# Kernel optimization log

Hardware: AMD Instinct MI355X
Metric: run time of the kernel (lower is better)

The kernel has to match this reference:

```python
import jax, jax.numpy as jnp
import numpy as np

B, T, S, H, E, V, NUM_OOV = 32, 32, 100, 512, 300, 45000, 10
INF = 1e12


def setup_inputs() -> dict:
    key = jax.random.key(0)
    ks = jax.random.split(key, 24)
    def n(k, shape, s=0.02):
        return jax.random.normal(k, shape, jnp.float32) * s
    return dict(
        trg_seq=jax.random.randint(ks[0], (B, T), 0, V),
        ext_src_seq=jax.random.randint(ks[1], (B, S), 0, V + NUM_OOV),
        h0=n(ks[2], (1, B, H), 0.1),
        c0=n(ks[3], (1, B, H), 0.1),
        tree_output=n(ks[4], (B, S, H), 1.0),
        tree_enc_states=n(ks[5], (1, B, H), 0.1),
        encoder_outputs=n(ks[6], (B, S, H), 1.0),
        encoder_mask=jnp.zeros((B, S), bool),
        embedding=n(ks[7], (V, E)),
        W_enc=n(ks[8], (2 * H, H)), b_enc=jnp.zeros((H,), jnp.float32),
        W_red=n(ks[9], (E + H, E)), b_red=jnp.zeros((E,), jnp.float32),
        W_ih=n(ks[10], (E, 4 * H)), W_hh=n(ks[11], (H, 4 * H)),
        b_ih=jnp.zeros((4 * H,), jnp.float32), b_hh=jnp.zeros((4 * H,), jnp.float32),
        W_cat=n(ks[12], (2 * H, H)), b_cat=jnp.zeros((H,), jnp.float32),
        W_out=n(ks[13], (H, V)), b_out=jnp.zeros((V,), jnp.float32),
    )


def reference(trg_seq, ext_src_seq, h0, c0, tree_output, tree_enc_states,
              encoder_outputs, encoder_mask, embedding, W_enc, b_enc,
              W_red, b_red, W_ih, W_hh, b_ih, b_hh, W_cat, b_cat, W_out, b_out):
    # encoder features: [B,S,2H] -> [B,S,H]
    memories = jnp.concatenate([tree_output, encoder_outputs], axis=-1) @ W_enc + b_enc
    rows = jnp.arange(B)[:, None]  # for per-row scatter-max
    Vext = V + NUM_OOV

    def step(carry, y):
        h, c, ctx = carry  # h,c: [B,H], ctx: [B,H]
        emb = embedding[y]                                   # [B,E]
        x = jnp.concatenate([emb, ctx], axis=-1) @ W_red + b_red  # [B,E]
        gates = x @ W_ih + h @ W_hh + (b_ih + b_hh)          # [B,4H]
        i, f, g, o = jnp.split(gates, 4, axis=-1)            # torch gate order i,f,g,o
        c_new = jax.nn.sigmoid(f) * c + jax.nn.sigmoid(i) * jnp.tanh(g)
        h_new = jax.nn.sigmoid(o) * jnp.tanh(c_new)
        energy = jnp.einsum('bh,bsh->bs', h_new, memories)   # [B,S]
        energy = jnp.where(encoder_mask, -INF, energy)
        attn = jax.nn.softmax(energy, axis=-1)
        ctx_new = jnp.einsum('bs,bsh->bh', attn, memories)   # [B,H]
        z = jnp.tanh(jnp.concatenate([h_new, ctx_new], axis=-1) @ W_cat + b_cat)
        logit = z @ W_out + b_out                            # [B,V]
        # pointer copy mechanism: scatter-max of energies into extended vocab
        ext = jnp.concatenate([logit, jnp.zeros((B, NUM_OOV), logit.dtype)], axis=-1)
        scat = jnp.full((B, Vext), -INF, logit.dtype).at[rows, ext_src_seq].max(energy)
        scat = jnp.where(scat == -INF, 0.0, scat)
        out = ext + scat
        out = jnp.where(out == 0.0, -INF, out)
        return (h_new, c_new, ctx_new), out

    init = (h0[0], c0[0], jnp.zeros((B, H), memories.dtype))
    _, logits = jax.lax.scan(step, init, trg_seq.T)  # [T,B,Vext]
    return jnp.transpose(logits, (1, 0, 2))          # [B,T,Vext]
```

## Files before the change

kernel.cpp:

```cpp
#include <hip/hip_runtime.h>
#include <hip/hip_bf16.h>
#include <stdint.h>

typedef __hip_bfloat16 bf16;
typedef __attribute__((ext_vector_type(8))) short short8;
typedef __attribute__((ext_vector_type(4))) float f32x4;

#define INFV 1e12f

constexpr int Vv = 45000;
constexpr int VE = 45010;

static __device__ __forceinline__ float bf2f(unsigned short u){
  union{ unsigned int i; float f; } w; w.i = ((unsigned int)u) << 16; return w.f;
}
static __device__ __forceinline__ unsigned short f2bf(float x){
  union { __hip_bfloat16 h; unsigned short u; } w; w.h = __float2bfloat16(x); return w.u;
}

template<bool ABF16, bool TANHOUT>
__launch_bounds__(256)
__global__ void k_gemm(const void* __restrict__ Ap, const void* __restrict__ Ap2, int Ksplit,
                       const float* __restrict__ Bp, const float* __restrict__ bias,
                       void* __restrict__ Cp, int M, int N, int K)
{
  __shared__ float As[16][68];
  __shared__ float Bs[16][68];
  int tid = threadIdx.x;
  int tx = tid & 15, ty = tid >> 4;
  int m0 = blockIdx.y * 64, n0 = blockIdx.x * 64;
  float acc[4][4] = {};
  for (int kc = 0; kc < K; kc += 16){
    for (int idx = tid; idx < 64*16; idx += 256){
      int r = idx >> 4, c = idx & 15;
      int gr = m0 + r, gk = kc + c;
      float v = 0.f;
      if (gr < M && gk < K){
        if (ABF16)            v = bf2f(((const unsigned short*)Ap)[(size_t)gr*K + gk]);
        else if (gk < Ksplit) v = ((const float*)Ap )[(size_t)gr*Ksplit + gk];
        else                  v = ((const float*)Ap2)[(size_t)gr*(K - Ksplit) + (gk - Ksplit)];
      }
      As[c][r] = v;
    }
    for (int idx = tid; idx < 16*64; idx += 256){
      int r = idx >> 6, c = idx & 63;
      int gk = kc + r, gn = n0 + c;
      Bs[r][c] = (gk < K && gn < N) ? Bp[(size_t)gk*N + gn] : 0.f;
    }
    __syncthreads();
    #pragma unroll
    for (int kk = 0; kk < 16; ++kk){
      float a[4], b[4];
      #pragma unroll
      for (int i = 0; i < 4; ++i) a[i] = As[kk][ty*4 + i];
      #pragma unroll
      for (int j = 0; j < 4; ++j) b[j] = Bs[kk][tx*4 + j];
      #pragma unroll
      for (int i = 0; i < 4; ++i)
        #pragma unroll
        for (int j = 0; j < 4; ++j) acc[i][j] = fmaf(a[i], b[j], acc[i][j]);
    }
    __syncthreads();
  }
  for (int i = 0; i < 4; ++i){
    int gr = m0 + ty*4 + i; if (gr >= M) continue;
    for (int j = 0; j < 4; ++j){
      int gn = n0 + tx*4 + j; if (gn >= N) continue;
      float v = acc[i][j] + (bias ? bias[gn] : 0.f);
      if (TANHOUT) ((unsigned short*)Cp)[(size_t)gr*N + gn] = f2bf(tanhf(v));
      else         ((float*)Cp)[(size_t)gr*N + gn] = v;
    }
  }
}

__global__ void k_cvt(const float* __restrict__ src, unsigned short* __restrict__ dst, int n){
  int i = blockIdx.x*256 + threadIdx.x;
  if (i < n) dst[i] = f2bf(src[i]);
}

__global__ void k_gather(const int* __restrict__ trg, const float* __restrict__ emb,
                         float* __restrict__ EmbA){
  int i = blockIdx.x*256 + threadIdx.x;
  if (i >= 1024*300) return;
  int r = i / 300, e = i - r*300;
  EmbA[i] = emb[(size_t)trg[r]*300 + e];
}

__global__ void k_bsum(const float* __restrict__ a, const float* __restrict__ b,
                       float* __restrict__ o){
  int i = blockIdx.x*256 + threadIdx.x;
  if (i < 2048) o[i] = a[i] + b[i];
}

__global__ void k_wgt(const float* __restrict__ Wf, const float* __restrict__ W_hh,
                      unsigned short* __restrict__ WgT){
  int idx = blockIdx.x*256 + threadIdx.x;
  if (idx >= 2048*1024) return;
  int cp = idx >> 10, k = idx & 1023;
  int c = (cp & 3)*512 + (cp >> 2);
  float v = (k < 512) ? Wf[(size_t)k*2048 + c] : W_hh[(size_t)(k-512)*2048 + c];
  WgT[idx] = f2bf(v);
}

__launch_bounds__(256)
__global__ void k_wot(const float* __restrict__ W_out, unsigned short* __restrict__ WoT){
  __shared__ float tl[64][65];
  int n0 = blockIdx.x * 64;
  int k0 = blockIdx.y * 64;
  int tid = threadIdx.x;
  for (int idx = tid; idx < 64*64; idx += 256){
    int r = idx >> 6, c = idx & 63;
    int gn = n0 + c;
    tl[r][c] = (gn < Vv) ? W_out[(size_t)(k0 + r)*Vv + gn] : 0.f;
  }
  __syncthreads();
  for (int idx = tid; idx < 64*64; idx += 256){
    int r = idx >> 6, c = idx & 63;
    WoT[(size_t)(n0 + r)*512 + k0 + c] = f2bf(tl[c][r]);
  }
}

__global__ void k_init(const float* __restrict__ h0, const float* __restrict__ c0,
                       unsigned short* __restrict__ HCa, float* __restrict__ Cst){
  int i = blockIdx.x*256 + threadIdx.x;
  if (i < 32*1024){
    int b = i >> 10, k = i & 1023;
    HCa[i] = (k < 512) ? f2bf(0.f) : f2bf(h0[b*512 + (k - 512)]);
  }
  if (i < 32*512) Cst[i] = c0[i];
}

__launch_bounds__(256, 1)
__global__ void k_gates(const unsigned short* __restrict__ WgT,
                        const unsigned short* __restrict__ HCprev,
                        unsigned short* __restrict__ HCnext,
                        float* __restrict__ C_state,
                        const float* __restrict__ G1,
                        unsigned short* __restrict__ HCz,
                        int t)
{
  __shared__ char Bsm[64*272];
  int tid = threadIdx.x;
  int lane = tid & 63, w2 = tid >> 6;
  int blk = blockIdx.x;
  int l15 = lane & 15, lh = lane >> 4;
  f32x4 zero = {0.f,0.f,0.f,0.f};
  f32x4 acc0 = zero, acc1 = zero;
  const char* Ab = (const char*)HCprev;

  for (int kc = 0; kc < 1024; kc += 128){
    #pragma unroll
    for (int call = 0; call < 4; ++call){
      int o = call*4096 + tid*16;
      int r = o >> 8, cb = o & 255;
      short8 v = *(const short8*)((const char*)WgT + (size_t)(blk*64 + r)*2048 + kc*2 + cb);
      *(short8*)(Bsm + r*272 + cb) = v;
    }
    __syncthreads();
    #pragma unroll
    for (int ks = 0; ks < 4; ++ks){
      short8 a0 = *(const short8*)(Ab + (size_t)l15*2048      + (kc + ks*32)*2 + lh*16);
      short8 a1 = *(const short8*)(Ab + (size_t)(l15+16)*2048 + (kc + ks*32)*2 + lh*16);
      int br = w2*16 + l15;
      short8 bfr = *(const short8*)(Bsm + br*272 + ks*64 + lh*16);
      acc0 = __builtin_amdgcn_mfma_f32_16x16x32_bf16(a0, bfr, acc0, 0, 0, 0);
      acc1 = __builtin_amdgcn_mfma_f32_16x16x32_bf16(a1, bfr, acc1, 0, 0, 0);
    }
    __syncthreads();
  }

  int cg = blk*64 + w2*16 + l15;
  int hfull = cg >> 2, q = cg & 3;
  #pragma unroll
  for (int f = 0; f < 2; ++f){
    #pragma unroll
    for (int j = 0; j < 4; ++j){
      int b = f*16 + 4*lh + j;
      float g = (f ? acc1[j] : acc0[j]) + G1[((size_t)b*32 + t)*2048 + q*512 + hfull];
      float x1 = (q == 2) ? tanhf(g) : 1.f/(1.f + expf(-g));
      float xg = __shfl_xor(x1, 2);
      float xf = __shfl_xor(x1, 1);
      float xo = __shfl_xor(x1, 3);
      if (q == 0){
        float co = C_state[b*512 + hfull];
        float cn = xf*co + x1*xg;
        float hn = xo * tanhf(cn);
        C_state[b*512 + hfull] = cn;
        unsigned short hb = f2bf(hn);
        HCnext[b*1024 + 512 + hfull] = hb;
        HCz[((size_t)b*32 + t)*1024 + hfull] = hb;
      }
    }
  }
}

__launch_bounds__(256, 1)
__global__ void k_attn(const unsigned short* __restrict__ memB,
                       const unsigned char* __restrict__ emask,
                       unsigned short* __restrict__ HCnext,
                       unsigned short* __restrict__ HCz,
                       float* __restrict__ Esave,
                       int t)
{
  int b = blockIdx.x;
  int tid = threadIdx.x, lane = tid & 63, w = tid >> 6;
  __shared__ float E_s[100];
  __shared__ float attn_s[100];
  float hreg[8];
  {
    short8 hv = *(const short8*)(HCnext + b*1024 + 512 + lane*8);
    #pragma unroll
    for (int i = 0; i < 8; ++i) hreg[i] = bf2f((unsigned short)hv[i]);
  }
  for (int s = w; s < 100; s += 4){
    short8 mv = *(const short8*)(memB + ((size_t)b*100 + s)*512 + lane*8);
    float a = 0.f;
    #pragma unroll
    for (int i = 0; i < 8; ++i) a = fmaf(hreg[i], bf2f((unsigned short)mv[i]), a);
    #pragma unroll
    for (int d = 1; d < 64; d <<= 1) a += __shfl_xor(a, d);
    if (lane == 0){
      float e = emask[b*100 + s] ? -INFV : a;
      E_s[s] = e;
      Esave[((size_t)b*32 + t)*100 + s] = e;
    }
  }
  __syncthreads();
  if (w == 0){
    float ea = (lane < 100) ? E_s[lane] : -INFV;
    float eb = (lane + 64 < 100) ? E_s[lane + 64] : -INFV;
    float m = fmaxf(ea, eb);
    #pragma unroll
    for (int d = 1; d < 64; d <<= 1) m = fmaxf(m, __shfl_xor(m, d));
    float p = ((lane < 100) ? expf(ea - m) : 0.f) + ((lane + 64 < 100) ? expf(eb - m) : 0.f);
    #pragma unroll
    for (int d = 1; d < 64; d <<= 1) p += __shfl_xor(p, d);
    float inv = 1.f / p;
    if (lane < 100)      attn_s[lane]      = expf(ea - m) * inv;
    if (lane + 64 < 100) attn_s[lane + 64] = expf(eb - m) * inv;
  }
  __syncthreads();
  for (int hh = tid; hh < 512; hh += 256){
    float a = 0.f;
    for (int s = 0; s < 100; ++s)
      a = fmaf(attn_s[s], bf2f(memB[((size_t)b*100 + s)*512 + hh]), a);
    unsigned short cbv = f2bf(a);
    HCnext[b*1024 + hh] = cbv;
    HCz[((size_t)b*32 + t)*1024 + 512 + hh] = cbv;
  }
}

__launch_bounds__(256, 2)
__global__ void k_logits(const unsigned short* __restrict__ Zbf,
                         const unsigned short* __restrict__ WoT,
                         const float* __restrict__ b_out,
                         const float* __restrict__ Esave,
                         const int* __restrict__ ext_src,
                         float* __restrict__ out)
{
  __shared__ char smem[128*128*4];
  char* smA = smem;
  char* smB = smem + 10240;
  int tid = threadIdx.x, lane = tid & 63;
  int w = tid >> 6, wr = w >> 1, wc = w & 1;
  int m0 = blockIdx.y * 128, n0 = blockIdx.x * 128;
  int l15 = lane & 15, lh = lane >> 4;
  f32x4 zero = {0.f,0.f,0.f,0.f};
  f32x4 acc[4][4];
  #pragma unroll
  for (int mi = 0; mi < 4; ++mi)
    #pragma unroll
    for (int ni = 0; ni < 4; ++ni) acc[mi][ni] = zero;

  for (int kc = 0; kc < 512; kc += 32){
    #pragma unroll
    for (int call = 0; call < 2; ++call){
      int o = call*4096 + tid*16;
      int r = o >> 6, cb = o & 63;
      short8 va = *(const short8*)((const char*)Zbf + (size_t)(m0 + r)*1024 + kc*2 + cb);
      *(short8*)(smA + r*80 + cb) = va;
      short8 vb = *(const short8*)((const char*)WoT + (size_t)(n0 + r)*1024 + kc*2 + cb);
      *(short8*)(smB + r*80 + cb) = vb;
    }
    __syncthreads();
    short8 af[4], bfv[4];
    #pragma unroll
    for (int mi = 0; mi < 4; ++mi) af[mi]  = *(const short8*)(smA + (wr*64 + mi*16 + l15)*80 + lh*16);
    #pragma unroll
    for (int ni = 0; ni < 4; ++ni) bfv[ni] = *(const short8*)(smB + (wc*64 + ni*16 + l15)*80 + lh*16);
    #pragma unroll
    for (int mi = 0; mi < 4; ++mi)
      #pragma unroll
      for (int ni = 0; ni < 4; ++ni)
        acc[mi][ni] = __builtin_amdgcn_mfma_f32_16x16x32_bf16(af[mi], bfv[ni], acc[mi][ni], 0, 0, 0);
    __syncthreads();
  }

  float* smax = (float*)smem;
  for (int i = tid; i < 128*128; i += 256) smax[i] = -INFV;
  __syncthreads();
  if (tid < 128){
    int rg = m0 + tid;
    int b = rg >> 5;
    const int* es = ext_src + b*100;
    const float* ev = Esave + (size_t)rg*100;
    float* row = smax + tid*128;
    for (int s = 0; s < 100; ++s){
      unsigned int d = (unsigned int)(es[s] - n0);
      if (d < 128u){
        float e = ev[s];
        if (e > -9e11f && e > row[d]) row[d] = e;
      }
    }
  }
  __syncthreads();

  #pragma unroll
  for (int mi = 0; mi < 4; ++mi){
    #pragma unroll
    for (int ni = 0; ni < 4; ++ni){
      #pragma unroll
      for (int j = 0; j < 4; ++j){
        int rl = wr*64 + mi*16 + 4*lh + j;
        int cl = wc*64 + ni*16 + l15;
        int cg = n0 + cl;
        if (cg < VE){
          float v = acc[mi][ni][j];
          float base = (cg < Vv) ? (v + b_out[cg]) : 0.f;
          float sm = smax[rl*128 + cl];
          float o = base + (sm > -9e11f ? sm : 0.f);
          if (o == 0.f) o = -INFV;
          out[(size_t)(m0 + rl)*VE + cg] = o;
        }
      }
    }
  }
}

extern "C" void kernel_launch(void* const* d_in, const int* in_sizes, int n_in,
                              void* d_out, int out_size, void* d_ws, size_t ws_size,
                              hipStream_t stream)
{
  const int*   trg    = (const int*)  d_in[0];
  const int*   ext    = (const int*)  d_in[1];
  const float* h0     = (const float*)d_in[2];
  const float* c0     = (const float*)d_in[3];
  const float* tree   = (const float*)d_in[4];
  const float* enc    = (const float*)d_in[6];
  const unsigned char* emask = (const unsigned char*)d_in[7];
  const float* emb    = (const float*)d_in[8];
  const float* W_enc  = (const float*)d_in[9];
  const float* b_enc  = (const float*)d_in[10];
  const float* W_red  = (const float*)d_in[11];
  const float* b_red  = (const float*)d_in[12];
  const float* W_ih   = (const float*)d_in[13];
  const float* W_hh   = (const float*)d_in[14];
  const float* b_ih   = (const float*)d_in[15];
  const float* b_hh   = (const float*)d_in[16];
  const float* W_cat  = (const float*)d_in[17];
  const float* b_cat  = (const float*)d_in[18];
  const float* W_out  = (const float*)d_in[19];
  const float* b_out  = (const float*)d_in[20];
  float* out = (float*)d_out;

  char* ws = (char*)d_ws;
  size_t off = 0;
  auto alloc = [&](size_t bytes)->char*{
    char* p = ws + off; off = (off + bytes + 255) & ~(size_t)255; return p;
  };
  float*          memf = (float*)         alloc(3200ull*512*4);
  unsigned short* memB = (unsigned short*)alloc(3200ull*512*2);
  float*          EmbA = (float*)         alloc(1024ull*300*4);
  float*          X0   = (float*)         alloc(1024ull*300*4);
  float*          G1   = (float*)         alloc(1024ull*2048*4);
  float*          bsum = (float*)         alloc(2048*4);
  float*          Wf   = (float*)         alloc(512ull*2048*4);
  unsigned short* WgT  = (unsigned short*)alloc(2048ull*1024*2);
  unsigned short* WoT  = (unsigned short*)alloc(45056ull*512*2);
  unsigned short* HCa  = (unsigned short*)alloc(32*1024*2);
  unsigned short* HCb  = (unsigned short*)alloc(32*1024*2);
  float*          Cst  = (float*)         alloc(32*512*4);
  unsigned short* HCz  = (unsigned short*)alloc(1024ull*1024*2);
  unsigned short* Zbf  = (unsigned short*)alloc(1024ull*512*2);
  float*          Esave= (float*)         alloc(1024ull*100*4);

  k_gemm<false,false><<<dim3(8,50), 256, 0, stream>>>(tree, enc, 512, W_enc, b_enc,
                                                      memf, 3200, 512, 1024);
  k_cvt<<<(3200*512 + 255)/256, 256, 0, stream>>>(memf, memB, 3200*512);

  k_gather<<<(1024*300 + 255)/256, 256, 0, stream>>>(trg, emb, EmbA);
  k_gemm<false,false><<<dim3(5,16), 256, 0, stream>>>(EmbA, nullptr, 300, W_red, b_red,
                                                      X0, 1024, 300, 300);
  k_bsum<<<8, 256, 0, stream>>>(b_ih, b_hh, bsum);
  k_gemm<false,false><<<dim3(32,16), 256, 0, stream>>>(X0, nullptr, 300, W_ih, bsum,
                                                       G1, 1024, 2048, 300);
  k_gemm<false,false><<<dim3(32,8), 256, 0, stream>>>(W_red + 300*300, nullptr, 300, W_ih,
                                                      nullptr, Wf, 512, 2048, 300);
  k_wgt<<<(2048*1024 + 255)/256, 256, 0, stream>>>(Wf, W_hh, WgT);
  k_wot<<<dim3(704,8), 256, 0, stream>>>(W_out, WoT);
  k_init<<<128, 256, 0, stream>>>(h0, c0, HCa, Cst);

  for (int t = 0; t < 32; ++t){
    unsigned short* hp = (t & 1) ? HCb : HCa;
    unsigned short* hn = (t & 1) ? HCa : HCb;
    k_gates<<<32, 256, 0, stream>>>(WgT, hp, hn, Cst, G1, HCz, t);
    k_attn <<<32, 256, 0, stream>>>(memB, emask, hn, HCz, Esave, t);
  }

  k_gemm<true,true><<<dim3(8,16), 256, 0, stream>>>(HCz, nullptr, 1024, W_cat, b_cat,
                                                    Zbf, 1024, 512, 1024);
  k_logits<<<dim3(352,8), 256, 0, stream>>>(Zbf, WoT, b_out, Esave, ext, out);
}
```

Baseline: 2.313 ms.

## Move prologue and W_cat GEMMs onto bf16 MFMA kernel and shrink logits LDS

```diff
diff --git a/kernel.cpp b/kernel.cpp
--- a/kernel.cpp
+++ b/kernel.cpp
@@ -18,72 +18,117 @@
   union { __hip_bfloat16 h; unsigned short u; } w; w.h = __float2bfloat16(x); return w.u;
 }
 
-template<bool ABF16, bool TANHOUT>
+__launch_bounds__(256, 2)
+__global__ void k_mm(const unsigned short* __restrict__ A, int lda,
+                     const unsigned short* __restrict__ B, int ldb, int NB,
+                     const float* __restrict__ bias,
+                     void* __restrict__ C, int ldc,
+                     int M, int N, int NZ, int K, int mode)
+{
+  __shared__ char smem[20480];
+  char* smA = smem;
+  char* smB = smem + 10240;
+  int tid = threadIdx.x, lane = tid & 63;
+  int w = tid >> 6, wr = w >> 1, wc = w & 1;
+  int m0 = blockIdx.y * 128, n0 = blockIdx.x * 128;
+  int l15 = lane & 15, lh = lane >> 4;
+  f32x4 zero = {0.f,0.f,0.f,0.f};
+  f32x4 acc[4][4];
+  #pragma unroll
+  for (int mi = 0; mi < 4; ++mi)
+    #pragma unroll
+    for (int ni = 0; ni < 4; ++ni) acc[mi][ni] = zero;
+  short8 z8 = {0,0,0,0,0,0,0,0};
+
+  for (int kc = 0; kc < K; kc += 32){
+    #pragma unroll
+    for (int call = 0; call < 2; ++call){
+      int o = call*4096 + tid*16;
+      int r = o >> 6, cb = o & 63;
+      short8 va = z8, vb = z8;
+      if (m0 + r < M)  va = *(const short8*)((const char*)A + ((size_t)(m0+r)*lda + kc)*2 + cb);
+      if (n0 + r < NB) vb = *(const short8*)((const char*)B + ((size_t)(n0+r)*ldb + kc)*2 + cb);
+      *(short8*)(smA + r*80 + cb) = va;
+      *(short8*)(smB + r*80 + cb) = vb;
+    }
+    __syncthreads();
+    short8 af[4], bfv[4];
+    #pragma unroll
+    for (int mi = 0; mi < 4; ++mi) af[mi]  = *(const short8*)(smA + (wr*64 + mi*16 + l15)*80 + lh*16);
+    #pragma unroll
+    for (int ni = 0; ni < 4; ++ni) bfv[ni] = *(const short8*)(smB + (wc*64 + ni*16 + l15)*80 + lh*16);
+    #pragma unroll
+    for (int mi = 0; mi < 4; ++mi)
+      #pragma unroll
+      for (int ni = 0; ni < 4; ++ni)
+        acc[mi][ni] = __builtin_amdgcn_mfma_f32_16x16x32_bf16(af[mi], bfv[ni], acc[mi][ni], 0, 0, 0);
+    __syncthreads();
+  }
+
+  #pragma unroll
+  for (int mi = 0; mi < 4; ++mi){
+    #pragma unroll
+    for (int ni = 0; ni < 4; ++ni){
+      #pragma unroll
+      for (int j = 0; j < 4; ++j){
+        int gr = m0 + wr*64 + mi*16 + 4*lh + j;
+        int cg = n0 + wc*64 + ni*16 + l15;
+        if (gr < M && cg < NZ){
+          float v = (cg < N) ? acc[mi][ni][j] + (bias ? bias[cg] : 0.f) : 0.f;
+          if (mode == 0) ((float*)C)[(size_t)gr*ldc + cg] = v;
+          else {
+            if (mode == 2) v = tanhf(v);
+            ((unsigned short*)C)[(size_t)gr*ldc + cg] = f2bf(v);
+          }
+        }
+      }
+    }
+  }
+}
+
 __launch_bounds__(256)
-__global__ void k_gemm(const void* __restrict__ Ap, const void* __restrict__ Ap2, int Ksplit,
-                       const float* __restrict__ Bp, const float* __restrict__ bias,
-                       void* __restrict__ Cp, int M, int N, int K)
-{
-  __shared__ float As[16][68];
-  __shared__ float Bs[16][68];
+__global__ void k_tbf(const float* __restrict__ in, int ldin,
+                      unsigned short* __restrict__ out,
+                      int K, int N, int K2, int N2)
+{
+  __shared__ float tl[64][65];
+  int n0 = blockIdx.x * 64, k0 = blockIdx.y * 64;
   int tid = threadIdx.x;
-  int tx = tid & 15, ty = tid >> 4;
-  int m0 = blockIdx.y * 64, n0 = blockIdx.x * 64;
-  float acc[4][4] = {};
-  for (int kc = 0; kc < K; kc += 16){
-    for (int idx = tid; idx < 64*16; idx += 256){
-      int r = idx >> 4, c = idx & 15;
-      int gr = m0 + r, gk = kc + c;
-      float v = 0.f;
-      if (gr < M && gk < K){
-        if (ABF16)            v = bf2f(((const unsigned short*)Ap)[(size_t)gr*K + gk]);
-        else if (gk < Ksplit) v = ((const float*)Ap )[(size_t)gr*Ksplit + gk];
-        else                  v = ((const float*)Ap2)[(size_t)gr*(K - Ksplit) + (gk - Ksplit)];
-      }
-      As[c][r] = v;
-    }
-    for (int idx = tid; idx < 16*64; idx += 256){
-      int r = idx >> 6, c = idx & 63;
-      int gk = kc + r, gn = n0 + c;
-      Bs[r][c] = (gk < K && gn < N) ? Bp[(size_t)gk*N + gn] : 0.f;
-    }
-    __syncthreads();
-    #pragma unroll
-    for (int kk = 0; kk < 16; ++kk){
-      float a[4], b[4];
-      #pragma unroll
-      for (int i = 0; i < 4; ++i) a[i] = As[kk][ty*4 + i];
-      #pragma unroll
-      for (int j = 0; j < 4; ++j) b[j] = Bs[kk][tx*4 + j];
-      #pragma unroll
-      for (int i = 0; i < 4; ++i)
-        #pragma unroll
-        for (int j = 0; j < 4; ++j) acc[i][j] = fmaf(a[i], b[j], acc[i][j]);
-    }
-    __syncthreads();
-  }
-  for (int i = 0; i < 4; ++i){
-    int gr = m0 + ty*4 + i; if (gr >= M) continue;
-    for (int j = 0; j < 4; ++j){
-      int gn = n0 + tx*4 + j; if (gn >= N) continue;
-      float v = acc[i][j] + (bias ? bias[gn] : 0.f);
-      if (TANHOUT) ((unsigned short*)Cp)[(size_t)gr*N + gn] = f2bf(tanhf(v));
-      else         ((float*)Cp)[(size_t)gr*N + gn] = v;
-    }
-  }
-}
-
-__global__ void k_cvt(const float* __restrict__ src, unsigned short* __restrict__ dst, int n){
+  for (int idx = tid; idx < 64*64; idx += 256){
+    int r = idx >> 6, c = idx & 63;
+    int gk = k0 + r, gn = n0 + c;
+    tl[r][c] = (gk < K && gn < N) ? in[(size_t)gk*ldin + gn] : 0.f;
+  }
+  __syncthreads();
+  for (int idx = tid; idx < 64*64; idx += 256){
+    int r = idx >> 6, c = idx & 63;
+    int gn = n0 + r, gk = k0 + c;
+    if (gn < N2 && gk < K2) out[(size_t)gn*K2 + gk] = f2bf(tl[c][r]);
+  }
+}
+
+__global__ void k_cat2bf(const float* __restrict__ tree, const float* __restrict__ enc,
+                         unsigned short* __restrict__ Acat){
   int i = blockIdx.x*256 + threadIdx.x;
-  if (i < n) dst[i] = f2bf(src[i]);
-}
-
-__global__ void k_gather(const int* __restrict__ trg, const float* __restrict__ emb,
-                         float* __restrict__ EmbA){
+  if (i >= 3200*1024) return;
+  int r = i >> 10, c = i & 1023;
+  float v = (c < 512) ? tree[(size_t)r*512 + c] : enc[(size_t)r*512 + (c - 512)];
+  Acat[i] = f2bf(v);
+}
+
+__global__ void k_gatherbf(const int* __restrict__ trg, const float* __restrict__ emb,
+                           unsigned short* __restrict__ EmbAb){
   int i = blockIdx.x*256 + threadIdx.x;
-  if (i >= 1024*300) return;
-  int r = i / 300, e = i - r*300;
-  EmbA[i] = emb[(size_t)trg[r]*300 + e];
+  if (i >= 1024*320) return;
+  int r = i / 320, c = i - r*320;
+  EmbAb[i] = (c < 300) ? f2bf(emb[(size_t)trg[r]*300 + c]) : (unsigned short)0;
+}
+
+__global__ void k_cvtpad(const float* __restrict__ in, unsigned short* __restrict__ out){
+  int i = blockIdx.x*256 + threadIdx.x;
+  if (i >= 512*320) return;
+  int r = i / 320, c = i - r*320;
+  out[i] = (c < 300) ? f2bf(in[(size_t)r*300 + c]) : (unsigned short)0;
 }
 
 __global__ void k_bsum(const float* __restrict__ a, const float* __restrict__ b,
@@ -100,24 +145,6 @@
   int c = (cp & 3)*512 + (cp >> 2);
   float v = (k < 512) ? Wf[(size_t)k*2048 + c] : W_hh[(size_t)(k-512)*2048 + c];
   WgT[idx] = f2bf(v);
-}
-
-__launch_bounds__(256)
-__global__ void k_wot(const float* __restrict__ W_out, unsigned short* __restrict__ WoT){
-  __shared__ float tl[64][65];
-  int n0 = blockIdx.x * 64;
-  int k0 = blockIdx.y * 64;
-  int tid = threadIdx.x;
-  for (int idx = tid; idx < 64*64; idx += 256){
-    int r = idx >> 6, c = idx & 63;
-    int gn = n0 + c;
-    tl[r][c] = (gn < Vv) ? W_out[(size_t)(k0 + r)*Vv + gn] : 0.f;
-  }
-  __syncthreads();
-  for (int idx = tid; idx < 64*64; idx += 256){
-    int r = idx >> 6, c = idx & 63;
-    WoT[(size_t)(n0 + r)*512 + k0 + c] = f2bf(tl[c][r]);
-  }
 }
 
 __global__ void k_init(const float* __restrict__ h0, const float* __restrict__ c0,
@@ -250,7 +277,7 @@
   }
 }
 
-__launch_bounds__(256, 2)
+__launch_bounds__(256, 4)
 __global__ void k_logits(const unsigned short* __restrict__ Zbf,
                          const unsigned short* __restrict__ WoT,
                          const float* __restrict__ b_out,
@@ -258,7 +285,7 @@
                          const int* __restrict__ ext_src,
                          float* __restrict__ out)
 {
-  __shared__ char smem[128*128*4];
+  __shared__ char smem[32768];
   char* smA = smem;
   char* smB = smem + 10240;
   int tid = threadIdx.x, lane = tid & 63;
@@ -297,43 +324,47 @@
   }
 
   float* smax = (float*)smem;
-  for (int i = tid; i < 128*128; i += 256) smax[i] = -INFV;
-  __syncthreads();
-  if (tid < 128){
-    int rg = m0 + tid;
-    int b = rg >> 5;
-    const int* es = ext_src + b*100;
-    const float* ev = Esave + (size_t)rg*100;
-    float* row = smax + tid*128;
-    for (int s = 0; s < 100; ++s){
-      unsigned int d = (unsigned int)(es[s] - n0);
-      if (d < 128u){
-        float e = ev[s];
-        if (e > -9e11f && e > row[d]) row[d] = e;
-      }
-    }
-  }
-  __syncthreads();
-
-  #pragma unroll
-  for (int mi = 0; mi < 4; ++mi){
-    #pragma unroll
-    for (int ni = 0; ni < 4; ++ni){
-      #pragma unroll
-      for (int j = 0; j < 4; ++j){
-        int rl = wr*64 + mi*16 + 4*lh + j;
-        int cl = wc*64 + ni*16 + l15;
-        int cg = n0 + cl;
-        if (cg < VE){
-          float v = acc[mi][ni][j];
-          float base = (cg < Vv) ? (v + b_out[cg]) : 0.f;
-          float sm = smax[rl*128 + cl];
-          float o = base + (sm > -9e11f ? sm : 0.f);
-          if (o == 0.f) o = -INFV;
-          out[(size_t)(m0 + rl)*VE + cg] = o;
+  for (int half = 0; half < 2; ++half){
+    for (int i = tid; i < 64*128; i += 256) smax[i] = -INFV;
+    __syncthreads();
+    if (tid < 64){
+      int rg = m0 + half*64 + tid;
+      int b = rg >> 5;
+      const int* es = ext_src + b*100;
+      const float* ev = Esave + (size_t)rg*100;
+      float* row = smax + tid*128;
+      for (int s = 0; s < 100; ++s){
+        unsigned int d = (unsigned int)(es[s] - n0);
+        if (d < 128u){
+          float e = ev[s];
+          if (e > -9e11f && e > row[d]) row[d] = e;
         }
       }
     }
+    __syncthreads();
+    if (wr == half){
+      #pragma unroll
+      for (int mi = 0; mi < 4; ++mi){
+        #pragma unroll
+        for (int ni = 0; ni < 4; ++ni){
+          #pragma unroll
+          for (int j = 0; j < 4; ++j){
+            int rll = mi*16 + 4*lh + j;
+            int cl = wc*64 + ni*16 + l15;
+            int cg = n0 + cl;
+            if (cg < VE){
+              float v = acc[mi][ni][j];
+              float base = (cg < Vv) ? (v + b_out[cg]) : 0.f;
+              float sm = smax[rll*128 + cl];
+              float o = base + (sm > -9e11f ? sm : 0.f);
+              if (o == 0.f) o = -INFV;
+              out[(size_t)(m0 + half*64 + rll)*VE + cg] = o;
+            }
+          }
+        }
+      }
+    }
+    __syncthreads();
   }
 }
 
@@ -368,36 +399,48 @@
   auto alloc = [&](size_t bytes)->char*{
     char* p = ws + off; off = (off + bytes + 255) & ~(size_t)255; return p;
   };
-  float*          memf = (float*)         alloc(3200ull*512*4);
-  unsigned short* memB = (unsigned short*)alloc(3200ull*512*2);
-  float*          EmbA = (float*)         alloc(1024ull*300*4);
-  float*          X0   = (float*)         alloc(1024ull*300*4);
-  float*          G1   = (float*)         alloc(1024ull*2048*4);
-  float*          bsum = (float*)         alloc(2048*4);
-  float*          Wf   = (float*)         alloc(512ull*2048*4);
-  unsigned short* WgT  = (unsigned short*)alloc(2048ull*1024*2);
-  unsigned short* WoT  = (unsigned short*)alloc(45056ull*512*2);
-  unsigned short* HCa  = (unsigned short*)alloc(32*1024*2);
-  unsigned short* HCb  = (unsigned short*)alloc(32*1024*2);
-  float*          Cst  = (float*)         alloc(32*512*4);
-  unsigned short* HCz  = (unsigned short*)alloc(1024ull*1024*2);
-  unsigned short* Zbf  = (unsigned short*)alloc(1024ull*512*2);
-  float*          Esave= (float*)         alloc(1024ull*100*4);
-
-  k_gemm<false,false><<<dim3(8,50), 256, 0, stream>>>(tree, enc, 512, W_enc, b_enc,
-                                                      memf, 3200, 512, 1024);
-  k_cvt<<<(3200*512 + 255)/256, 256, 0, stream>>>(memf, memB, 3200*512);
-
-  k_gather<<<(1024*300 + 255)/256, 256, 0, stream>>>(trg, emb, EmbA);
-  k_gemm<false,false><<<dim3(5,16), 256, 0, stream>>>(EmbA, nullptr, 300, W_red, b_red,
-                                                      X0, 1024, 300, 300);
+  unsigned short* Acat  = (unsigned short*)alloc(3200ull*1024*2);
+  unsigned short* WencT = (unsigned short*)alloc(512ull*1024*2);
+  unsigned short* memB  = (unsigned short*)alloc(3200ull*512*2);
+  unsigned short* EmbAb = (unsigned short*)alloc(1024ull*320*2);
+  unsigned short* WredT1= (unsigned short*)alloc(320ull*320*2);
+  unsigned short* X0b   = (unsigned short*)alloc(1024ull*320*2);
+  unsigned short* WihT  = (unsigned short*)alloc(2048ull*320*2);
+  float*          G1    = (float*)         alloc(1024ull*2048*4);
+  float*          bsum  = (float*)         alloc(2048*4);
+  unsigned short* Wred2b= (unsigned short*)alloc(512ull*320*2);
+  unsigned short* WgT   = (unsigned short*)alloc(2048ull*1024*2);
+  unsigned short* WoT   = (unsigned short*)alloc(45056ull*512*2);
+  unsigned short* WcatT = (unsigned short*)alloc(512ull*1024*2);
+  unsigned short* HCa   = (unsigned short*)alloc(32*1024*2);
+  unsigned short* HCb   = (unsigned short*)alloc(32*1024*2);
+  float*          Cst   = (float*)         alloc(32*512*4);
+  unsigned short* HCz   = (unsigned short*)alloc(1024ull*1024*2);
+  unsigned short* Zbf   = (unsigned short*)alloc(1024ull*512*2);
+  float*          Esave = (float*)         alloc(1024ull*100*4);
+  float*          Wf    = (float*)Acat;
+
+  k_cat2bf<<<12800, 256, 0, stream>>>(tree, enc, Acat);
+  k_tbf<<<dim3(8,16), 256, 0, stream>>>(W_enc, 512, WencT, 1024, 512, 1024, 512);
+  k_mm<<<dim3(4,25), 256, 0, stream>>>(Acat, 1024, WencT, 1024, 512, b_enc,
+                                       memB, 512, 3200, 512, 512, 1024, 1);
+
+  k_gatherbf<<<1280, 256, 0, stream>>>(trg, emb, EmbAb);
+  k_tbf<<<dim3(5,5), 256, 0, stream>>>(W_red, 300, WredT1, 300, 300, 320, 320);
+  k_tbf<<<dim3(32,5), 256, 0, stream>>>(W_ih, 2048, WihT, 300, 2048, 320, 2048);
   k_bsum<<<8, 256, 0, stream>>>(b_ih, b_hh, bsum);
-  k_gemm<false,false><<<dim3(32,16), 256, 0, stream>>>(X0, nullptr, 300, W_ih, bsum,
-                                                       G1, 1024, 2048, 300);
-  k_gemm<false,false><<<dim3(32,8), 256, 0, stream>>>(W_red + 300*300, nullptr, 300, W_ih,
-                                                      nullptr, Wf, 512, 2048, 300);
-  k_wgt<<<(2048*1024 + 255)/256, 256, 0, stream>>>(Wf, W_hh, WgT);
-  k_wot<<<dim3(704,8), 256, 0, stream>>>(W_out, WoT);
+  k_mm<<<dim3(3,8), 256, 0, stream>>>(EmbAb, 320, WredT1, 320, 320, b_red,
+                                      X0b, 320, 1024, 300, 320, 320, 1);
+  k_mm<<<dim3(16,8), 256, 0, stream>>>(X0b, 320, WihT, 320, 2048, bsum,
+                                       G1, 2048, 1024, 2048, 2048, 320, 0);
+
+  k_cvtpad<<<640, 256, 0, stream>>>(W_red + 300*300, Wred2b);
+  k_mm<<<dim3(16,4), 256, 0, stream>>>(Wred2b, 320, WihT, 320, 2048, nullptr,
+                                       Wf, 2048, 512, 2048, 2048, 320, 0);
+  k_wgt<<<8192, 256, 0, stream>>>(Wf, W_hh, WgT);
+
+  k_tbf<<<dim3(704,8), 256, 0, stream>>>(W_out, 45000, WoT, 512, 45000, 512, 45056);
+  k_tbf<<<dim3(8,16), 256, 0, stream>>>(W_cat, 512, WcatT, 1024, 512, 1024, 512);
   k_init<<<128, 256, 0, stream>>>(h0, c0, HCa, Cst);
 
   for (int t = 0; t < 32; ++t){
@@ -407,7 +450,7 @@
     k_attn <<<32, 256, 0, stream>>>(memB, emask, hn, HCz, Esave, t);
   }
 
-  k_gemm<true,true><<<dim3(8,16), 256, 0, stream>>>(HCz, nullptr, 1024, W_cat, b_cat,
-                                                    Zbf, 1024, 512, 1024);
+  k_mm<<<dim3(4,8), 256, 0, stream>>>(HCz, 1024, WcatT, 1024, 512, b_cat,
+                                      Zbf, 512, 1024, 512, 512, 1024, 2);
   k_logits<<<dim3(352,8), 256, 0, stream>>>(Zbf, WoT, b_out, Esave, ext, out);
 }
```

Result: faster. 1.952 ms (-15.6%).
